# Kernel optimization log

Measured on AMD Instinct MI355X. Metric: run time of the kernel, lower is better.

Reference implementation:

```python
import jax, jax.numpy as jnp
import numpy as np

D_DIM = 128
K_DIM = 32


def setup_inputs() -> dict:
    key = jax.random.key(0)
    k1, k2, k3 = jax.random.split(key, 3)
    B, H, W = 8, 64, 64
    std1 = 1.0 / (K_DIM * D_DIM) ** 0.5
    std2 = 1.0 / K_DIM ** 0.5
    X = jax.random.normal(k1, (B, D_DIM, H, W), dtype=jnp.float32)
    codewords = jax.random.uniform(k2, (K_DIM, D_DIM), dtype=jnp.float32, minval=-std1, maxval=std1)
    scale = jax.random.uniform(k3, (K_DIM,), dtype=jnp.float32, minval=-std2, maxval=std2)
    return {"X": X, "codewords": codewords, "scale": scale}


def reference(X, codewords, scale):
    # X: [B, D, H, W] -> descriptors [B, N, D]
    B, D, H, W = X.shape
    Xf = X.reshape(B, D, H * W).transpose(0, 2, 1)  # [B, N, D]
    # Squared distance ||x - c||^2 expanded: avoids materializing [B,N,K,D]
    x_sq = jnp.sum(Xf * Xf, axis=-1, keepdims=True)          # [B, N, 1]
    c_sq = jnp.sum(codewords * codewords, axis=-1)           # [K]
    cross = jnp.einsum('bnd,kd->bnk', Xf, codewords)         # [B, N, K]
    dist2 = x_sq - 2.0 * cross + c_sq                        # [B, N, K]
    # NOTE: faithful to source -- softmax over scale * dist^2 (no negation)
    A = jax.nn.softmax(dist2 * scale, axis=-1)               # [B, N, K]
    # E[b,k,d] = sum_n A[b,n,k] * (x[b,n,d] - c[k,d])
    E = jnp.einsum('bnk,bnd->bkd', A, Xf) - jnp.sum(A, axis=1)[..., None] * codewords
    return E  # [B, K, D]
```

## Files before the change

### kernel.cpp

```cpp
#include <hip/hip_runtime.h>
#include <hip/hip_bf16.h>

#define D_DIM 128
#define K_DIM 32
#define NPIX  4096
#define TPB   128

typedef __bf16 bf16x8 __attribute__((ext_vector_type(8)));
typedef unsigned short u16x8 __attribute__((ext_vector_type(8)));
typedef float f32x4 __attribute__((ext_vector_type(4)));

__device__ __forceinline__ unsigned short f2bf(float f) {
    union { float f; unsigned u; } v; v.f = f;
    unsigned r = v.u + 0x7FFFu + ((v.u >> 16) & 1u);
    return (unsigned short)(r >> 16);
}
__device__ __forceinline__ unsigned pack2(float lo, float hi) {
    __hip_bfloat162 h = __float22bfloat162_rn(make_float2(lo, hi));
    union { __hip_bfloat162 b; unsigned u; } u; u.b = h;
    return u.u;
}
__device__ __forceinline__ float bf2f(unsigned short u) {
    union { unsigned u; float f; } v; v.u = ((unsigned)u) << 16;
    return v.f;
}
__device__ __forceinline__ bf16x8 ldfrag(const unsigned short* p) {
    union { u16x8 s; bf16x8 b; } u;
    u.s = *(const u16x8*)p;
    return u.b;
}
__device__ __forceinline__ bf16x8 pack8(float4 a, float4 b) {
    union { unsigned d[4]; bf16x8 v; } u;
    u.d[0] = pack2(a.x, a.y); u.d[1] = pack2(a.z, a.w);
    u.d[2] = pack2(b.x, b.y); u.d[3] = pack2(b.z, b.w);
    return u.v;
}

#define XND_LD 136
#define CW_LD  136
#define SA_LD  136

__global__ __launch_bounds__(512) void enc_kernel(
    const float* __restrict__ X,
    const float* __restrict__ cw,
    const float* __restrict__ scale,
    float* __restrict__ ws)
{
    __shared__ __align__(16) unsigned short sXnd[TPB * XND_LD];
    __shared__ __align__(16) unsigned short sCW[K_DIM * CW_LD];
    __shared__ __align__(16) unsigned short sA[K_DIM * SA_LD];
    __shared__ float sXsqP[16 * 129];
    __shared__ float sXsq[TPB];
    __shared__ float sSum[K_DIM];
    __shared__ float sSc[K_DIM];
    __shared__ float sCS[K_DIM];

    const int ltid = threadIdx.x;
    const int b    = blockIdx.x >> 5;
    const int n0   = (blockIdx.x & 31) * TPB;
    const int lane = ltid & 63;
    const int w    = ltid >> 6;
    const int l15  = lane & 15;
    const int quad = lane >> 4;

    if (ltid < K_DIM) {
        const float4* cr = (const float4*)(cw + ltid * D_DIM);
        float cs = 0.f;
        #pragma unroll 8
        for (int q = 0; q < 32; ++q) {
            float4 c4 = cr[q];
            cs = fmaf(c4.x, c4.x, fmaf(c4.y, c4.y, fmaf(c4.z, c4.z, fmaf(c4.w, c4.w, cs))));
        }
        float s = scale[ltid];
        sSc[ltid] = s;
        sCS[ltid] = cs * s;
        sSum[ltid] = 0.f;
    }

    {
        const int r  = ltid >> 4;
        const int q8 = ltid & 15;
        float4 c0 = *(const float4*)(cw + r * D_DIM + 8 * q8);
        float4 c1 = *(const float4*)(cw + r * D_DIM + 8 * q8 + 4);
        uint4 pk;
        pk.x = pack2(c0.x, c0.y); pk.y = pack2(c0.z, c0.w);
        pk.z = pack2(c1.x, c1.y); pk.w = pack2(c1.z, c1.w);
        *(uint4*)&sCW[r * CW_LD + 8 * q8] = pk;
    }

    {
        const int c   = ltid & 15;
        const int rp  = (ltid >> 4) & 3;
        const int ph  = ltid >> 6;
        const int pxh = (ph & 1) * 64;
        const int dbl = (ph >> 1) * 16;
        float px[4] = {0.f, 0.f, 0.f, 0.f};
        const float* xb = X + (size_t)b * D_DIM * NPIX + n0 + pxh;
        #pragma unroll
        for (int p = 0; p < 4; ++p) {
            const int pair = rp + 4 * p + dbl;
            const int d0   = 2 * pair;
            float4 f0 = *(const float4*)(xb + (size_t)d0 * NPIX + 4 * c);
            float4 f1 = *(const float4*)(xb + (size_t)(d0 + 1) * NPIX + 4 * c);
            px[0] = fmaf(f0.x, f0.x, fmaf(f1.x, f1.x, px[0]));
            px[1] = fmaf(f0.y, f0.y, fmaf(f1.y, f1.y, px[1]));
            px[2] = fmaf(f0.z, f0.z, fmaf(f1.z, f1.z, px[2]));
            px[3] = fmaf(f0.w, f0.w, fmaf(f1.w, f1.w, px[3]));
            const int pix = pxh + 4 * c;
            *(unsigned*)&sXnd[(pix + 0) * XND_LD + d0] = pack2(f0.x, f1.x);
            *(unsigned*)&sXnd[(pix + 1) * XND_LD + d0] = pack2(f0.y, f1.y);
            *(unsigned*)&sXnd[(pix + 2) * XND_LD + d0] = pack2(f0.z, f1.z);
            *(unsigned*)&sXnd[(pix + 3) * XND_LD + d0] = pack2(f0.w, f1.w);
        }
        const int row = rp + 4 * (ph >> 1);
        #pragma unroll
        for (int j = 0; j < 4; ++j) sXsqP[row * 129 + pxh + 4 * c + j] = px[j];
    }

    float4 g[4][2];
    {
        const int d = 16 * w + l15;
        const float* xrow = X + ((size_t)b * D_DIM + d) * NPIX + n0;
        #pragma unroll
        for (int ks = 0; ks < 4; ++ks) {
            const float* p = xrow + 8 * quad + 32 * ks;
            g[ks][0] = *(const float4*)p;
            g[ks][1] = *(const float4*)(p + 4);
        }
    }
    __syncthreads();

    if (ltid < TPB) {
        float s = 0.f;
        #pragma unroll
        for (int r = 0; r < 16; ++r) s += sXsqP[r * 129 + ltid];
        sXsq[ltid] = s;
    }

    f32x4 accA[2] = {{0.f, 0.f, 0.f, 0.f}, {0.f, 0.f, 0.f, 0.f}};
    {
        const int prow = (16 * w + l15) * XND_LD;
        #pragma unroll
        for (int ks = 0; ks < 4; ++ks) {
            const int off = 8 * quad + 32 * ks;
            bf16x8 bfrag = ldfrag(&sXnd[prow + off]);
            bf16x8 a0 = ldfrag(&sCW[l15 * CW_LD + off]);
            bf16x8 a1 = ldfrag(&sCW[(l15 + 16) * CW_LD + off]);
            accA[0] = __builtin_amdgcn_mfma_f32_16x16x32_bf16(a0, bfrag, accA[0], 0, 0, 0);
            accA[1] = __builtin_amdgcn_mfma_f32_16x16x32_bf16(a1, bfrag, accA[1], 0, 0, 0);
        }
    }
    __syncthreads();

    {
        const float xsq = sXsq[16 * w + l15];
        float e8[8];
        float psum = 0.f;
        #pragma unroll
        for (int mt = 0; mt < 2; ++mt)
            #pragma unroll
            for (int reg = 0; reg < 4; ++reg) {
                const int k = 16 * mt + 4 * quad + reg;
                float l = fmaf(sSc[k], fmaf(-2.f, accA[mt][reg], xsq), sCS[k]);
                float e = __expf(l);
                e8[4 * mt + reg] = e;
                psum += e;
            }
        psum += __shfl_xor(psum, 16);
        psum += __shfl_xor(psum, 32);
        const float inv = 1.f / psum;
        float r8[8];
        #pragma unroll
        for (int i = 0; i < 8; ++i) {
            e8[i] *= inv;
            r8[i] = e8[i];
        }
        #pragma unroll
        for (int mt = 0; mt < 2; ++mt)
            #pragma unroll
            for (int reg = 0; reg < 4; ++reg) {
                const int k = 16 * mt + 4 * quad + reg;
                sA[k * SA_LD + 16 * w + l15] = f2bf(e8[4 * mt + reg]);
            }
        #pragma unroll
        for (int i = 0; i < 8; ++i) {
            r8[i] += __shfl_xor(r8[i], 1);
            r8[i] += __shfl_xor(r8[i], 2);
            r8[i] += __shfl_xor(r8[i], 4);
            r8[i] += __shfl_xor(r8[i], 8);
        }
        if (l15 == 0) {
            #pragma unroll
            for (int mt = 0; mt < 2; ++mt)
                #pragma unroll
                for (int reg = 0; reg < 4; ++reg)
                    atomicAdd(&sSum[16 * mt + 4 * quad + reg], r8[4 * mt + reg]);
        }
    }
    __syncthreads();

    f32x4 accE[2] = {{0.f, 0.f, 0.f, 0.f}, {0.f, 0.f, 0.f, 0.f}};
    {
        #pragma unroll
        for (int ks = 0; ks < 4; ++ks) {
            const int off = 8 * quad + 32 * ks;
            bf16x8 bfrag = pack8(g[ks][0], g[ks][1]);
            bf16x8 a0 = ldfrag(&sA[l15 * SA_LD + off]);
            bf16x8 a1 = ldfrag(&sA[(l15 + 16) * SA_LD + off]);
            accE[0] = __builtin_amdgcn_mfma_f32_16x16x32_bf16(a0, bfrag, accE[0], 0, 0, 0);
            accE[1] = __builtin_amdgcn_mfma_f32_16x16x32_bf16(a1, bfrag, accE[1], 0, 0, 0);
        }
    }

    {
        float* wsl = ws + (size_t)blockIdx.x * (K_DIM * D_DIM);
        const int d = 16 * w + l15;
        #pragma unroll
        for (int mt = 0; mt < 2; ++mt) {
            #pragma unroll
            for (int reg = 0; reg < 4; ++reg) {
                const int k = 16 * mt + 4 * quad + reg;
                float sk  = sSum[k];
                float cwv = bf2f(sCW[k * CW_LD + d]);
                wsl[k * D_DIM + d] = fmaf(-sk, cwv, accE[mt][reg]);
            }
        }
    }
}

__global__ __launch_bounds__(64) void reduce_kernel(
    const float4* __restrict__ ws, float4* __restrict__ out)
{
    const int tid = blockIdx.x * 64 + threadIdx.x;
    const int b   = tid >> 10;
    const int r   = tid & 1023;
    const float4* p = ws + (size_t)b * 32 * 1024 + r;
    float4 s = make_float4(0.f, 0.f, 0.f, 0.f);
    #pragma unroll
    for (int t = 0; t < 32; ++t) {
        float4 v = p[(size_t)t * 1024];
        s.x += v.x; s.y += v.y; s.z += v.z; s.w += v.w;
    }
    out[tid] = s;
}

extern "C" void kernel_launch(void* const* d_in, const int* in_sizes, int n_in,
                              void* d_out, int out_size, void* d_ws, size_t ws_size,
                              hipStream_t stream) {
    const float* X  = (const float*)d_in[0];
    const float* cw = (const float*)d_in[1];
    const float* sc = (const float*)d_in[2];
    float* out = (float*)d_out;
    (void)in_sizes; (void)n_in; (void)ws_size; (void)out_size;

    hipLaunchKernelGGL(enc_kernel, dim3(256), dim3(512), 0, stream,
                       X, cw, sc, (float*)d_ws);
    hipLaunchKernelGGL(reduce_kernel, dim3(128), dim3(64), 0, stream,
                       (const float4*)d_ws, (float4*)out);
}
```

Measured before the change: 73.31 us.

## Halve pixel tile, stage X in both layouts in LDS instead of reloading

Each block now covers 64 pixels with 256 threads, and 512 blocks are launched. X is read from global memory once and written into LDS in two bf16 layouts: pixel-major for the distance MFMA and channel-major for the aggregation MFMA. This removes the second global read of X that the old code kept in registers, and the softmax buffer shares LDS with the x-squared partials. In exchange each block writes twice as many partial results to the workspace, so the reduce kernel has to sum 64 partials per output instead of 32.

```diff
diff --git a/kernel.cpp b/kernel.cpp
--- a/kernel.cpp
+++ b/kernel.cpp
@@ -4,7 +4,9 @@
 #define D_DIM 128
 #define K_DIM 32
 #define NPIX  4096
-#define TPB   128
+#define TPB   64
+#define NTILE 64
+#define NBLK  512
 
 typedef __bf16 bf16x8 __attribute__((ext_vector_type(8)));
 typedef unsigned short u16x8 __attribute__((ext_vector_type(8)));
@@ -29,37 +31,35 @@
     u.s = *(const u16x8*)p;
     return u.b;
 }
-__device__ __forceinline__ bf16x8 pack8(float4 a, float4 b) {
-    union { unsigned d[4]; bf16x8 v; } u;
-    u.d[0] = pack2(a.x, a.y); u.d[1] = pack2(a.z, a.w);
-    u.d[2] = pack2(b.x, b.y); u.d[3] = pack2(b.z, b.w);
-    return u.v;
-}
 
 #define XND_LD 136
+#define XDN_LD 72
 #define CW_LD  136
-#define SA_LD  136
-
-__global__ __launch_bounds__(512) void enc_kernel(
+#define SA_LD  72
+
+__global__ __launch_bounds__(256) void enc_kernel(
     const float* __restrict__ X,
     const float* __restrict__ cw,
     const float* __restrict__ scale,
     float* __restrict__ ws)
 {
     __shared__ __align__(16) unsigned short sXnd[TPB * XND_LD];
+    __shared__ __align__(16) unsigned short sXdn[D_DIM * XDN_LD];
     __shared__ __align__(16) unsigned short sCW[K_DIM * CW_LD];
-    __shared__ __align__(16) unsigned short sA[K_DIM * SA_LD];
-    __shared__ float sXsqP[16 * 129];
+    __shared__ __align__(16) unsigned char sPool[K_DIM * SA_LD * 2];
     __shared__ float sXsq[TPB];
     __shared__ float sSum[K_DIM];
     __shared__ float sSc[K_DIM];
     __shared__ float sCS[K_DIM];
 
+    unsigned short* sA    = (unsigned short*)sPool;
+    float*          sXsqP = (float*)sPool;
+
     const int ltid = threadIdx.x;
-    const int b    = blockIdx.x >> 5;
-    const int n0   = (blockIdx.x & 31) * TPB;
+    const int b    = blockIdx.x >> 6;
+    const int n0   = (blockIdx.x & 63) * TPB;
     const int lane = ltid & 63;
-    const int w    = ltid >> 6;
+    const int wv   = ltid >> 6;
     const int l15  = lane & 15;
     const int quad = lane >> 4;
 
@@ -78,68 +78,62 @@
     }
 
     {
-        const int r  = ltid >> 4;
-        const int q8 = ltid & 15;
-        float4 c0 = *(const float4*)(cw + r * D_DIM + 8 * q8);
-        float4 c1 = *(const float4*)(cw + r * D_DIM + 8 * q8 + 4);
-        uint4 pk;
-        pk.x = pack2(c0.x, c0.y); pk.y = pack2(c0.z, c0.w);
-        pk.z = pack2(c1.x, c1.y); pk.w = pack2(c1.z, c1.w);
-        *(uint4*)&sCW[r * CW_LD + 8 * q8] = pk;
-    }
-
-    {
-        const int c   = ltid & 15;
-        const int rp  = (ltid >> 4) & 3;
-        const int ph  = ltid >> 6;
-        const int pxh = (ph & 1) * 64;
-        const int dbl = (ph >> 1) * 16;
+        const int r  = ltid >> 3;
+        const int q8 = ltid & 7;
+        const float* crow = cw + r * D_DIM + 16 * q8;
+        float4 c0 = *(const float4*)(crow);
+        float4 c1 = *(const float4*)(crow + 4);
+        float4 c2 = *(const float4*)(crow + 8);
+        float4 c3 = *(const float4*)(crow + 12);
+        uint4 p0, p1;
+        p0.x = pack2(c0.x, c0.y); p0.y = pack2(c0.z, c0.w);
+        p0.z = pack2(c1.x, c1.y); p0.w = pack2(c1.z, c1.w);
+        p1.x = pack2(c2.x, c2.y); p1.y = pack2(c2.z, c2.w);
+        p1.z = pack2(c3.x, c3.y); p1.w = pack2(c3.z, c3.w);
+        *(uint4*)&sCW[r * CW_LD + 16 * q8]     = p0;
+        *(uint4*)&sCW[r * CW_LD + 16 * q8 + 8] = p1;
+    }
+
+    {
+        const int c  = ltid & 15;
+        const int rp = ltid >> 4;
         float px[4] = {0.f, 0.f, 0.f, 0.f};
-        const float* xb = X + (size_t)b * D_DIM * NPIX + n0 + pxh;
+        const float* xb = X + (size_t)b * D_DIM * NPIX + n0;
         #pragma unroll
         for (int p = 0; p < 4; ++p) {
-            const int pair = rp + 4 * p + dbl;
-            const int d0   = 2 * pair;
+            const int d0 = 2 * (rp + 16 * p);
             float4 f0 = *(const float4*)(xb + (size_t)d0 * NPIX + 4 * c);
             float4 f1 = *(const float4*)(xb + (size_t)(d0 + 1) * NPIX + 4 * c);
             px[0] = fmaf(f0.x, f0.x, fmaf(f1.x, f1.x, px[0]));
             px[1] = fmaf(f0.y, f0.y, fmaf(f1.y, f1.y, px[1]));
             px[2] = fmaf(f0.z, f0.z, fmaf(f1.z, f1.z, px[2]));
             px[3] = fmaf(f0.w, f0.w, fmaf(f1.w, f1.w, px[3]));
-            const int pix = pxh + 4 * c;
+            const int pix = 4 * c;
             *(unsigned*)&sXnd[(pix + 0) * XND_LD + d0] = pack2(f0.x, f1.x);
             *(unsigned*)&sXnd[(pix + 1) * XND_LD + d0] = pack2(f0.y, f1.y);
             *(unsigned*)&sXnd[(pix + 2) * XND_LD + d0] = pack2(f0.z, f1.z);
             *(unsigned*)&sXnd[(pix + 3) * XND_LD + d0] = pack2(f0.w, f1.w);
-        }
-        const int row = rp + 4 * (ph >> 1);
-        #pragma unroll
-        for (int j = 0; j < 4; ++j) sXsqP[row * 129 + pxh + 4 * c + j] = px[j];
-    }
-
-    float4 g[4][2];
-    {
-        const int d = 16 * w + l15;
-        const float* xrow = X + ((size_t)b * D_DIM + d) * NPIX + n0;
-        #pragma unroll
-        for (int ks = 0; ks < 4; ++ks) {
-            const float* p = xrow + 8 * quad + 32 * ks;
-            g[ks][0] = *(const float4*)p;
-            g[ks][1] = *(const float4*)(p + 4);
-        }
+            uint2 t0, t1;
+            t0.x = pack2(f0.x, f0.y); t0.y = pack2(f0.z, f0.w);
+            t1.x = pack2(f1.x, f1.y); t1.y = pack2(f1.z, f1.w);
+            *(uint2*)&sXdn[(d0    ) * XDN_LD + 4 * c] = t0;
+            *(uint2*)&sXdn[(d0 + 1) * XDN_LD + 4 * c] = t1;
+        }
+        #pragma unroll
+        for (int j = 0; j < 4; ++j) sXsqP[rp * 65 + 4 * c + j] = px[j];
     }
     __syncthreads();
 
     if (ltid < TPB) {
         float s = 0.f;
         #pragma unroll
-        for (int r = 0; r < 16; ++r) s += sXsqP[r * 129 + ltid];
+        for (int r = 0; r < 16; ++r) s += sXsqP[r * 65 + ltid];
         sXsq[ltid] = s;
     }
 
     f32x4 accA[2] = {{0.f, 0.f, 0.f, 0.f}, {0.f, 0.f, 0.f, 0.f}};
     {
-        const int prow = (16 * w + l15) * XND_LD;
+        const int prow = (16 * wv + l15) * XND_LD;
         #pragma unroll
         for (int ks = 0; ks < 4; ++ks) {
             const int off = 8 * quad + 32 * ks;
@@ -153,7 +147,7 @@
     __syncthreads();
 
     {
-        const float xsq = sXsq[16 * w + l15];
+        const float xsq = sXsq[16 * wv + l15];
         float e8[8];
         float psum = 0.f;
         #pragma unroll
@@ -180,7 +174,7 @@
             #pragma unroll
             for (int reg = 0; reg < 4; ++reg) {
                 const int k = 16 * mt + 4 * quad + reg;
-                sA[k * SA_LD + 16 * w + l15] = f2bf(e8[4 * mt + reg]);
+                sA[k * SA_LD + 16 * wv + l15] = f2bf(e8[4 * mt + reg]);
             }
         #pragma unroll
         for (int i = 0; i < 8; ++i) {
@@ -199,45 +193,53 @@
     }
     __syncthreads();
 
-    f32x4 accE[2] = {{0.f, 0.f, 0.f, 0.f}, {0.f, 0.f, 0.f, 0.f}};
-    {
-        #pragma unroll
-        for (int ks = 0; ks < 4; ++ks) {
+    f32x4 accE[2][2] = {{{0.f,0.f,0.f,0.f},{0.f,0.f,0.f,0.f}},
+                        {{0.f,0.f,0.f,0.f},{0.f,0.f,0.f,0.f}}};
+    {
+        #pragma unroll
+        for (int ks = 0; ks < 2; ++ks) {
             const int off = 8 * quad + 32 * ks;
-            bf16x8 bfrag = pack8(g[ks][0], g[ks][1]);
             bf16x8 a0 = ldfrag(&sA[l15 * SA_LD + off]);
             bf16x8 a1 = ldfrag(&sA[(l15 + 16) * SA_LD + off]);
-            accE[0] = __builtin_amdgcn_mfma_f32_16x16x32_bf16(a0, bfrag, accE[0], 0, 0, 0);
-            accE[1] = __builtin_amdgcn_mfma_f32_16x16x32_bf16(a1, bfrag, accE[1], 0, 0, 0);
+            #pragma unroll
+            for (int dt = 0; dt < 2; ++dt) {
+                const int d = 32 * wv + 16 * dt + l15;
+                bf16x8 bfrag = ldfrag(&sXdn[d * XDN_LD + off]);
+                accE[0][dt] = __builtin_amdgcn_mfma_f32_16x16x32_bf16(a0, bfrag, accE[0][dt], 0, 0, 0);
+                accE[1][dt] = __builtin_amdgcn_mfma_f32_16x16x32_bf16(a1, bfrag, accE[1][dt], 0, 0, 0);
+            }
         }
     }
 
     {
         float* wsl = ws + (size_t)blockIdx.x * (K_DIM * D_DIM);
-        const int d = 16 * w + l15;
         #pragma unroll
         for (int mt = 0; mt < 2; ++mt) {
             #pragma unroll
-            for (int reg = 0; reg < 4; ++reg) {
-                const int k = 16 * mt + 4 * quad + reg;
-                float sk  = sSum[k];
-                float cwv = bf2f(sCW[k * CW_LD + d]);
-                wsl[k * D_DIM + d] = fmaf(-sk, cwv, accE[mt][reg]);
-            }
-        }
-    }
-}
-
-__global__ __launch_bounds__(64) void reduce_kernel(
+            for (int dt = 0; dt < 2; ++dt) {
+                #pragma unroll
+                for (int reg = 0; reg < 4; ++reg) {
+                    const int k = 16 * mt + 4 * quad + reg;
+                    const int d = 32 * wv + 16 * dt + l15;
+                    float sk  = sSum[k];
+                    float cwv = bf2f(sCW[k * CW_LD + d]);
+                    wsl[k * D_DIM + d] = fmaf(-sk, cwv, accE[mt][dt][reg]);
+                }
+            }
+        }
+    }
+}
+
+__global__ __launch_bounds__(256) void reduce_kernel(
     const float4* __restrict__ ws, float4* __restrict__ out)
 {
-    const int tid = blockIdx.x * 64 + threadIdx.x;
+    const int tid = blockIdx.x * 256 + threadIdx.x;
     const int b   = tid >> 10;
     const int r   = tid & 1023;
-    const float4* p = ws + (size_t)b * 32 * 1024 + r;
+    const float4* p = ws + (size_t)b * NTILE * 1024 + r;
     float4 s = make_float4(0.f, 0.f, 0.f, 0.f);
     #pragma unroll
-    for (int t = 0; t < 32; ++t) {
+    for (int t = 0; t < NTILE; ++t) {
         float4 v = p[(size_t)t * 1024];
         s.x += v.x; s.y += v.y; s.z += v.z; s.w += v.w;
     }
@@ -253,8 +255,8 @@
     float* out = (float*)d_out;
     (void)in_sizes; (void)n_in; (void)ws_size; (void)out_size;
 
-    hipLaunchKernelGGL(enc_kernel, dim3(256), dim3(512), 0, stream,
+    hipLaunchKernelGGL(enc_kernel, dim3(NBLK), dim3(256), 0, stream,
                        X, cw, sc, (float*)d_ws);
-    hipLaunchKernelGGL(reduce_kernel, dim3(128), dim3(64), 0, stream,
+    hipLaunchKernelGGL(reduce_kernel, dim3(32), dim3(256), 0, stream,
                        (const float4*)d_ws, (float4*)out);
 }
```

Result: slower. 75.43 us (+2.9%).
